# Kernel optimization log

Measured on AMD Instinct MI355X. Metric: run time of the kernel, lower is better.

Reference implementation:

```python
import jax, jax.numpy as jnp
import numpy as np

B, S, D = 4, 4096, 256


def setup_inputs() -> dict:
    key = jax.random.key(0)
    ks = jax.random.split(key, 7)
    s = 1.0 / np.sqrt(D)
    return {
        "x": jax.random.normal(ks[0], (B, S, D), dtype=jnp.float32),
        "Wq": jax.random.normal(ks[1], (D, D), dtype=jnp.float32) * s,
        "bq": jax.random.normal(ks[2], (D,), dtype=jnp.float32) * s,
        "Wk": jax.random.normal(ks[3], (D, D), dtype=jnp.float32) * s,
        "bk": jax.random.normal(ks[4], (D,), dtype=jnp.float32) * s,
        "Wv": jax.random.normal(ks[5], (D, D), dtype=jnp.float32) * s,
        "bv": jax.random.normal(ks[6], (D,), dtype=jnp.float32) * s,
    }


def reference(x, Wq, bq, Wk, bk, Wv, bv):
    # QKV projections (torch Linear: y = x @ W^T + b; here W stored as [in, out])
    Q = jax.nn.relu(jnp.einsum("bsd,df->bsf", x, Wq) + bq)  # [B,S,D]
    K = jax.nn.relu(jnp.einsum("bsd,df->bsf", x, Wk) + bk)  # [B,S,D]
    V = jnp.einsum("bsd,df->bsf", x, Wv) + bv               # [B,S,D]
    scores = jnp.einsum("bqd,bkd->bqk", Q, K)               # [B,S,S], no 1/sqrt(d) scaling (as in source)
    attn = jax.nn.softmax(scores, axis=-1)
    return jnp.einsum("bqk,bkd->bqd", attn, V)              # [B,S,D]
```

## Files before the change

kernel.cpp:

```cpp
#include <hip/hip_runtime.h>
#include <stdint.h>

typedef __bf16 bf16;
typedef bf16 bf16x8 __attribute__((ext_vector_type(8)));
typedef _Float16 f16;
typedef f16 f16x8 __attribute__((ext_vector_type(8)));
typedef f16 f16x4 __attribute__((ext_vector_type(4)));
typedef float f32x4 __attribute__((ext_vector_type(4)));
typedef float f32x16 __attribute__((ext_vector_type(16)));
typedef unsigned short u16;
typedef unsigned int u32;
typedef u32 u32x2 __attribute__((ext_vector_type(2)));
typedef u16 u16x8v __attribute__((ext_vector_type(8)));

__device__ __forceinline__ u16 f2bf(float f) {
  u32 u = __float_as_uint(f);
  u32 r = u + 0x7fffu + ((u >> 16) & 1u);
  return (u16)(r >> 16);
}
__device__ __forceinline__ float bf2f(u16 h) { return __uint_as_float(((u32)h) << 16); }

__device__ __forceinline__ u32 pkrtz(float a, float b) {
  auto r = __builtin_amdgcn_cvt_pkrtz(a, b);
  u32 u; __builtin_memcpy(&u, &r, 4);
  return u;
}

union ABu { u16x8v u; bf16x8 b; };
union PAu { u32 w[4]; f16x8 v; };

__global__ void wt_kernel(const float* __restrict__ Wq, const float* __restrict__ Wk,
                          const float* __restrict__ Wv, u16* __restrict__ Wh,
                          u16* __restrict__ Wl) {
  int w = blockIdx.x >> 4;
  int chunk = blockIdx.x & 15;
  const float* W = (w == 0) ? Wq : (w == 1) ? Wk : Wv;
  int t = threadIdx.x;
  int o = chunk * 16 + (t & 15);
  int i0 = (t >> 4) * 16;
  u16x8v h0, h1, l0, l1;
  #pragma unroll
  for (int ii = 0; ii < 8; ++ii) {
    float v0 = W[(size_t)(i0 + ii) * 256 + o];
    u16 h = f2bf(v0); h0[ii] = h; l0[ii] = f2bf(v0 - bf2f(h));
    float v1 = W[(size_t)(i0 + 8 + ii) * 256 + o];
    h = f2bf(v1); h1[ii] = h; l1[ii] = f2bf(v1 - bf2f(h));
  }
  size_t base = (size_t)w * 65536 + (size_t)o * 256 + i0;
  *(u16x8v*)(Wh + base) = h0; *(u16x8v*)(Wh + base + 8) = h1;
  *(u16x8v*)(Wl + base) = l0; *(u16x8v*)(Wl + base + 8) = l1;
}

__global__ __launch_bounds__(256, 2) void proj_kernel(
    const float* __restrict__ x, const float* __restrict__ bq,
    const float* __restrict__ bk, const float* __restrict__ bv,
    const u16* __restrict__ Wh, const u16* __restrict__ Wl,
    f16* __restrict__ Qf, f16* __restrict__ Kf, f16* __restrict__ Vt) {
  __shared__ __align__(16) char Whs[16384];
  __shared__ __align__(16) char Wls[16384];

  int m = blockIdx.x, w = blockIdx.y;
  int tid = threadIdx.x, lane = tid & 63, wv = tid >> 6;
  int r = lane & 15, c = lane >> 4;
  int row0 = m * 128 + wv * 32;
  const char* Whw = (const char*)(Wh + (size_t)w * 65536);
  const char* Wlw = (const char*)(Wl + (size_t)w * 65536);
  const float* bias = (w == 0) ? bq : (w == 1) ? bk : bv;

  f32x4 acc[2][16];
  #pragma unroll
  for (int g = 0; g < 2; ++g)
    #pragma unroll
    for (int n = 0; n < 16; ++n) acc[g][n] = (f32x4)0.0f;

  for (int ks = 0; ks < 8; ++ks) {
    if (ks) __syncthreads();
    #pragma unroll
    for (int ss = 0; ss < 4; ++ss) {
      int slot = ss * 256 + tid;
      int row = slot >> 2, c4 = slot & 3;
      int dby = (c4 << 4) ^ (((row >> 1) & 3) << 4);
      const char* gh = Whw + (size_t)row * 512 + ks * 64 + dby;
      const char* gl = Wlw + (size_t)row * 512 + ks * 64 + dby;
      __builtin_amdgcn_global_load_lds(
          (const __attribute__((address_space(1))) void*)gh,
          (__attribute__((address_space(3))) void*)(Whs + slot * 16), 16, 0, 0);
      __builtin_amdgcn_global_load_lds(
          (const __attribute__((address_space(1))) void*)gl,
          (__attribute__((address_space(3))) void*)(Wls + slot * 16), 16, 0, 0);
    }
    __syncthreads();

    ABu ah[2], al[2];
    #pragma unroll
    for (int g = 0; g < 2; ++g) {
      const float* xrow = x + (size_t)(row0 + g * 16 + r) * 256 + ks * 32 + c * 8;
      float4 a0 = *(const float4*)(xrow);
      float4 a1 = *(const float4*)(xrow + 4);
      float xv[8] = {a0.x, a0.y, a0.z, a0.w, a1.x, a1.y, a1.z, a1.w};
      #pragma unroll
      for (int j = 0; j < 8; ++j) {
        u16 h = f2bf(xv[j]);
        ah[g].u[j] = h;
        al[g].u[j] = f2bf(xv[j] - bf2f(h));
      }
    }
    #pragma unroll
    for (int n = 0; n < 16; ++n) {
      int wrow = n * 16 + r;
      int wof = (c * 16) ^ (((wrow >> 1) & 3) << 4);
      bf16x8 whf = *(const bf16x8*)(Whs + wrow * 64 + wof);
      bf16x8 wlf = *(const bf16x8*)(Wls + wrow * 64 + wof);
      #pragma unroll
      for (int g = 0; g < 2; ++g) {
        acc[g][n] = __builtin_amdgcn_mfma_f32_16x16x32_bf16(ah[g].b, whf, acc[g][n], 0, 0, 0);
        acc[g][n] = __builtin_amdgcn_mfma_f32_16x16x32_bf16(al[g].b, whf, acc[g][n], 0, 0, 0);
        acc[g][n] = __builtin_amdgcn_mfma_f32_16x16x32_bf16(ah[g].b, wlf, acc[g][n], 0, 0, 0);
      }
    }
  }

  if (w < 2) {
    f16* outp = (w == 0) ? Qf : Kf;
    #pragma unroll
    for (int g = 0; g < 2; ++g)
      #pragma unroll
      for (int n = 0; n < 16; ++n) {
        int col = n * 16 + r;
        float bb = bias[col];
        #pragma unroll
        for (int i = 0; i < 4; ++i) {
          float v = fmaxf(acc[g][n][i] + bb, 0.0f);
          outp[(size_t)(row0 + g * 16 + c * 4 + i) * 256 + col] = (f16)v;
        }
      }
  } else {
    #pragma unroll
    for (int g = 0; g < 2; ++g) {
      int grow = row0 + g * 16 + c * 4;
      int b = grow >> 12, s0 = grow & 4095;
      #pragma unroll
      for (int n = 0; n < 16; ++n) {
        int d = n * 16 + r;
        float bb = bias[d];
        f16x4 pk;
        #pragma unroll
        for (int i = 0; i < 4; ++i) pk[i] = (f16)(acc[g][n][i] + bb);
        *(f16x4*)(Vt + (size_t)(b * 256 + d) * 4096 + s0) = pk;
      }
    }
  }
}

__global__ __launch_bounds__(256, 2) void attn_kernel(
    const f16* __restrict__ Qf, const f16* __restrict__ Kf,
    const f16* __restrict__ Vt, f16* __restrict__ Opart, float* __restrict__ Ml) {
  __shared__ __align__(16) char Ksm[2][16384];
  __shared__ __align__(16) char Vsm[3][16384];

  int bid = blockIdx.x;
  int xcd = bid & 7;
  int batch = xcd >> 1;
  int kq = ((xcd & 1) << 1) | ((bid >> 3) & 1);
  int qtl = bid >> 4;
  int tid = threadIdx.x, lane = tid & 63, wv = tid >> 6;
  int ln = lane & 31, hi = lane >> 5;
  int q0 = qtl * 128 + wv * 32;
  int kv0 = kq * 1024;

  f16x8 qf[16];
  {
    const f16* qp = Qf + ((size_t)(batch * 4096 + q0 + ln)) * 256 + hi * 8;
    #pragma unroll
    for (int ks = 0; ks < 16; ++ks) qf[ks] = *(const f16x8*)(qp + ks * 16);
  }

  f32x16 O[8];
  #pragma unroll
  for (int dt = 0; dt < 8; ++dt) O[dt] = (f32x16)0.0f;
  float m_ = -1.0e30f, l_ = 0.0f;
  PAu pa0_, pa1_;

  const char* Kbase = (const char*)(Kf + ((size_t)(batch * 4096 + kv0)) * 256);
  const char* Vbase = (const char*)(Vt + (size_t)batch * 1048576 + kv0);

#define STAGE(T, KB, VB)                                                       \
  {                                                                            \
    _Pragma("unroll")                                                          \
    for (int rr = 0; rr < 4; ++rr) {                                           \
      int slot = rr * 256 + tid;                                               \
      int krow = slot >> 5;                                                    \
      int dby = ((slot & 31) << 4) ^ ((krow & 7) << 4);                        \
      const char* g = Kbase + (size_t)((T) * 32 + krow) * 512 + dby;           \
      __builtin_amdgcn_global_load_lds(                                        \
          (const __attribute__((address_space(1))) void*)g,                    \
          (__attribute__((address_space(3))) void*)(Ksm[KB] + slot * 16), 16, 0, 0); \
    }                                                                          \
    _Pragma("unroll")                                                          \
    for (int rr = 0; rr < 4; ++rr) {                                           \
      int slot = rr * 256 + tid;                                               \
      int vrow = slot >> 2;                                                    \
      int dby = ((slot & 3) << 4) ^ (((vrow >> 1) & 3) << 4);                  \
      const char* g = Vbase + (size_t)vrow * 8192 + (T) * 64 + dby;            \
      __builtin_amdgcn_global_load_lds(                                        \
          (const __attribute__((address_space(1))) void*)g,                    \
          (__attribute__((address_space(3))) void*)(Vsm[VB] + slot * 16), 16, 0, 0); \
    }                                                                          \
  }

  int kswz = (ln & 7) << 4;
  int vswz = ((ln >> 1) & 3) << 4;
  int hi16 = hi * 16;

#define QKPV(T, DOPV)                                                          \
  {                                                                            \
    const char* Kc = Ksm[(T) & 1];                                             \
    const char* Vc = Vsm[((T) + 2) % 3];                                       \
    f32x16 sA = (f32x16)0.0f;                                                  \
    __builtin_amdgcn_s_setprio(1);                                             \
    _Pragma("unroll")                                                          \
    for (int ks = 0; ks < 16; ++ks) {                                          \
      f16x8 kf = *(const f16x8*)(Kc + ln * 512 + ((ks * 32 + hi16) ^ kswz));   \
      sA = __builtin_amdgcn_mfma_f32_32x32x16_f16(kf, qf[ks], sA, 0, 0, 0);    \
      if (DOPV) {                                                              \
        int dt = ks >> 1, half = ks & 1;                                       \
        f16x8 vf = *(const f16x8*)(Vc + (dt * 32 + ln) * 64 +                  \
                                   ((half * 32 + hi16) ^ vswz));               \
        O[dt] = __builtin_amdgcn_mfma_f32_32x32x16_f16(                        \
            half ? pa1_.v : pa0_.v, vf, O[dt], 0, 0, 0);                       \
      }                                                                        \
    }                                                                          \
    __builtin_amdgcn_s_setprio(0);                                             \
    float pm = fmaxf(                                                          \
        fmaxf(fmaxf(fmaxf(sA[0], sA[1]), fmaxf(sA[2], sA[3])),                 \
              fmaxf(fmaxf(sA[4], sA[5]), fmaxf(sA[6], sA[7]))),                \
        fmaxf(fmaxf(fmaxf(sA[8], sA[9]), fmaxf(sA[10], sA[11])),               \
              fmaxf(fmaxf(sA[12], sA[13]), fmaxf(sA[14], sA[15]))));           \
    pm = fmaxf(pm, __shfl_xor(pm, 32));                                        \
    if (!__all(pm <= m_ + 8.0f)) {                                             \
      float mn = fmaxf(m_, pm);                                                \
      float sc = __expf(m_ - mn);                                              \
      m_ = mn; l_ *= sc;                                                       \
      _Pragma("unroll")                                                        \
      for (int rg = 0; rg < 16; ++rg) {                                        \
        float srg = __shfl(sc, (rg & 3) + 8 * (rg >> 2) + 4 * hi);             \
        _Pragma("unroll")                                                      \
        for (int dt = 0; dt < 8; ++dt) O[dt][rg] *= srg;                       \
      }                                                                        \
    }                                                                          \
    float p_[16];                                                              \
    _Pragma("unroll")                                                          \
    for (int j = 0; j < 16; ++j) p_[j] = __expf(sA[j] - m_);                   \
    float ps = (((p_[0] + p_[1]) + (p_[2] + p_[3])) +                          \
                ((p_[4] + p_[5]) + (p_[6] + p_[7]))) +                         \
               (((p_[8] + p_[9]) + (p_[10] + p_[11])) +                        \
                ((p_[12] + p_[13]) + (p_[14] + p_[15])));                      \
    ps += __shfl_xor(ps, 32);                                                  \
    l_ += ps;                                                                  \
    {                                                                          \
      u32x2 r1 = __builtin_amdgcn_permlane32_swap(pkrtz(p_[0], p_[1]), pkrtz(p_[4], p_[5]), false, false); \
      u32x2 r2 = __builtin_amdgcn_permlane32_swap(pkrtz(p_[2], p_[3]), pkrtz(p_[6], p_[7]), false, false); \
      pa0_.w[0] = r1[0]; pa0_.w[1] = r2[0]; pa0_.w[2] = r1[1]; pa0_.w[3] = r2[1]; \
      u32x2 r3 = __builtin_amdgcn_permlane32_swap(pkrtz(p_[8], p_[9]), pkrtz(p_[12], p_[13]), false, false); \
      u32x2 r4 = __builtin_amdgcn_permlane32_swap(pkrtz(p_[10], p_[11]), pkrtz(p_[14], p_[15]), false, false); \
      pa1_.w[0] = r3[0]; pa1_.w[1] = r4[0]; pa1_.w[2] = r3[1]; pa1_.w[3] = r4[1]; \
    }                                                                          \
  }

  STAGE(0, 0, 0);
  STAGE(1, 1, 1);
  asm volatile("s_waitcnt vmcnt(8)" ::: "memory");
  __builtin_amdgcn_sched_barrier(0);
  __builtin_amdgcn_s_barrier();
  QKPV(0, false);

  for (int t = 1; t < 32; ++t) {
    __builtin_amdgcn_s_barrier();
    if (t < 31) {
      int kb = (t + 1) & 1, vb = (t + 1) % 3;
      STAGE(t + 1, kb, vb);
      asm volatile("s_waitcnt vmcnt(8)" ::: "memory");
    } else {
      asm volatile("s_waitcnt vmcnt(0)" ::: "memory");
    }
    __builtin_amdgcn_sched_barrier(0);
    __builtin_amdgcn_s_barrier();
    QKPV(t, true);
  }

  {
    const char* Vc = Vsm[31 % 3];
    #pragma unroll
    for (int ks = 0; ks < 16; ++ks) {
      int dt = ks >> 1, half = ks & 1;
      f16x8 vf = *(const f16x8*)(Vc + (dt * 32 + ln) * 64 + ((half * 32 + hi16) ^ vswz));
      O[dt] = __builtin_amdgcn_mfma_f32_32x32x16_f16(half ? pa1_.v : pa0_.v, vf, O[dt], 0, 0, 0);
    }
  }

  float invl = 1.0f / l_;
  #pragma unroll
  for (int rg = 0; rg < 16; ++rg) {
    int qr = (rg & 3) + 8 * (rg >> 2) + 4 * hi;
    float iv = __shfl(invl, qr);
    size_t row = (size_t)kq * 16384 + batch * 4096 + q0 + qr;
    #pragma unroll
    for (int dt = 0; dt < 8; ++dt)
      Opart[row * 256 + dt * 32 + ln] = (f16)(O[dt][rg] * iv);
  }
  if (hi == 0) {
    size_t grow = (size_t)kq * 16384 + batch * 4096 + q0 + ln;
    Ml[grow * 2] = m_;
    Ml[grow * 2 + 1] = l_;
  }
#undef STAGE
#undef QKPV
}

__global__ __launch_bounds__(256) void merge_kernel(
    const f16* __restrict__ Opart, const float* __restrict__ Ml,
    float* __restrict__ out) {
  int gid = blockIdx.x * 256 + threadIdx.x;
  int row = gid >> 5, d0 = (gid & 31) * 8;
  float m[4], l[4];
  #pragma unroll
  for (int p = 0; p < 4; ++p) {
    m[p] = Ml[((size_t)p * 16384 + row) * 2];
    l[p] = Ml[((size_t)p * 16384 + row) * 2 + 1];
  }
  float M = fmaxf(fmaxf(m[0], m[1]), fmaxf(m[2], m[3]));
  float wl[4], L = 0.f;
  #pragma unroll
  for (int p = 0; p < 4; ++p) { wl[p] = __expf(m[p] - M) * l[p]; L += wl[p]; }
  float o[8] = {0.f, 0.f, 0.f, 0.f, 0.f, 0.f, 0.f, 0.f};
  #pragma unroll
  for (int p = 0; p < 4; ++p) {
    f16x8 v = *(const f16x8*)(Opart + ((size_t)p * 16384 + row) * 256 + d0);
    #pragma unroll
    for (int j = 0; j < 8; ++j) o[j] += wl[p] * (float)v[j];
  }
  float invL = 1.0f / L;
  float4 o0 = {o[0] * invL, o[1] * invL, o[2] * invL, o[3] * invL};
  float4 o1 = {o[4] * invL, o[5] * invL, o[6] * invL, o[7] * invL};
  *(float4*)(out + (size_t)row * 256 + d0) = o0;
  *(float4*)(out + (size_t)row * 256 + d0 + 4) = o1;
}

extern "C" void kernel_launch(void* const* d_in, const int* in_sizes, int n_in,
                              void* d_out, int out_size, void* d_ws, size_t ws_size,
                              hipStream_t stream) {
  const float* x  = (const float*)d_in[0];
  const float* Wq = (const float*)d_in[1];
  const float* bq = (const float*)d_in[2];
  const float* Wk = (const float*)d_in[3];
  const float* bk = (const float*)d_in[4];
  const float* Wv = (const float*)d_in[5];
  const float* bv = (const float*)d_in[6];
  float* out = (float*)d_out;

  u16* Wh = (u16*)d_ws;
  u16* Wl = Wh + 3 * 65536;
  f16* Qf = (f16*)(Wl + 3 * 65536);
  f16* Kf = Qf + (size_t)16384 * 256;
  f16* Vt = Kf + (size_t)16384 * 256;
  f16* Opart = Vt + (size_t)4 * 256 * 4096;
  float* Ml = (float*)(Opart + (size_t)4 * 16384 * 256);

  wt_kernel<<<48, 256, 0, stream>>>(Wq, Wk, Wv, Wh, Wl);
  proj_kernel<<<dim3(128, 3), 256, 0, stream>>>(x, bq, bk, bv, Wh, Wl, Qf, Kf, Vt);
  attn_kernel<<<512, 256, 0, stream>>>(Qf, Kf, Vt, Opart, Ml);
  merge_kernel<<<2048, 256, 0, stream>>>(Opart, Ml, out);
}
```

Before: 168.2 us.

## Enlarge attention blocks to 8 waves with 64-key tiles and double buffering

The attention kernel now launches 256 blocks of 512 threads, each covering 256 query rows and sharing 64-key K/V tiles in LDS. This halves the number of barriers and stages per key range. The V buffers change from triple to double buffering with a new 128-byte row swizzle. Within each tile, the two 32-key halves are software pipelined, so the PV MMA of the first half is interleaved with the QK MMA of the second half. The cost is twice the LDS per block (128KB) and fewer, larger blocks, which may reduce occupancy and overlap across the CUs.

Measured after the change: 157.4 us. 1.07x faster.

```diff
diff --git a/kernel.cpp b/kernel.cpp
--- a/kernel.cpp
+++ b/kernel.cpp
@@ -152,11 +152,11 @@
   }
 }
 
-__global__ __launch_bounds__(256, 2) void attn_kernel(
+__global__ __launch_bounds__(512, 2) void attn_kernel(
     const f16* __restrict__ Qf, const f16* __restrict__ Kf,
     const f16* __restrict__ Vt, f16* __restrict__ Opart, float* __restrict__ Ml) {
-  __shared__ __align__(16) char Ksm[2][16384];
-  __shared__ __align__(16) char Vsm[3][16384];
+  __shared__ __align__(16) char Ksm[2][32768];
+  __shared__ __align__(16) char Vsm[2][32768];
 
   int bid = blockIdx.x;
   int xcd = bid & 7;
@@ -165,7 +165,7 @@
   int qtl = bid >> 4;
   int tid = threadIdx.x, lane = tid & 63, wv = tid >> 6;
   int ln = lane & 31, hi = lane >> 5;
-  int q0 = qtl * 128 + wv * 32;
+  int q0 = qtl * 256 + wv * 32;
   int kv0 = kq * 1024;
 
   f16x8 qf[16];
@@ -179,63 +179,45 @@
   #pragma unroll
   for (int dt = 0; dt < 8; ++dt) O[dt] = (f32x16)0.0f;
   float m_ = -1.0e30f, l_ = 0.0f;
-  PAu pa0_, pa1_;
 
   const char* Kbase = (const char*)(Kf + ((size_t)(batch * 4096 + kv0)) * 256);
   const char* Vbase = (const char*)(Vt + (size_t)batch * 1048576 + kv0);
 
-#define STAGE(T, KB, VB)                                                       \
+#define STAGE(T, BF)                                                           \
   {                                                                            \
     _Pragma("unroll")                                                          \
     for (int rr = 0; rr < 4; ++rr) {                                           \
-      int slot = rr * 256 + tid;                                               \
+      int slot = rr * 512 + tid;                                               \
       int krow = slot >> 5;                                                    \
       int dby = ((slot & 31) << 4) ^ ((krow & 7) << 4);                        \
-      const char* g = Kbase + (size_t)((T) * 32 + krow) * 512 + dby;           \
+      const char* g = Kbase + (size_t)((T) * 64 + krow) * 512 + dby;           \
       __builtin_amdgcn_global_load_lds(                                        \
           (const __attribute__((address_space(1))) void*)g,                    \
-          (__attribute__((address_space(3))) void*)(Ksm[KB] + slot * 16), 16, 0, 0); \
+          (__attribute__((address_space(3))) void*)(Ksm[BF] + slot * 16), 16, 0, 0); \
     }                                                                          \
     _Pragma("unroll")                                                          \
     for (int rr = 0; rr < 4; ++rr) {                                           \
-      int slot = rr * 256 + tid;                                               \
-      int vrow = slot >> 2;                                                    \
-      int dby = ((slot & 3) << 4) ^ (((vrow >> 1) & 3) << 4);                  \
-      const char* g = Vbase + (size_t)vrow * 8192 + (T) * 64 + dby;            \
+      int slot = rr * 512 + tid;                                               \
+      int vrow = slot >> 3;                                                    \
+      int dby = ((slot & 7) << 4) ^ ((vrow & 7) << 4);                         \
+      const char* g = Vbase + (size_t)vrow * 8192 + (T) * 128 + dby;           \
       __builtin_amdgcn_global_load_lds(                                        \
           (const __attribute__((address_space(1))) void*)g,                    \
-          (__attribute__((address_space(3))) void*)(Vsm[VB] + slot * 16), 16, 0, 0); \
+          (__attribute__((address_space(3))) void*)(Vsm[BF] + slot * 16), 16, 0, 0); \
     }                                                                          \
   }
 
   int kswz = (ln & 7) << 4;
-  int vswz = ((ln >> 1) & 3) << 4;
+  int vswz = (ln & 7) << 4;
   int hi16 = hi * 16;
 
-#define QKPV(T, DOPV)                                                          \
+#define SOFTMAX(SA, PA0, PA1)                                                  \
   {                                                                            \
-    const char* Kc = Ksm[(T) & 1];                                             \
-    const char* Vc = Vsm[((T) + 2) % 3];                                       \
-    f32x16 sA = (f32x16)0.0f;                                                  \
-    __builtin_amdgcn_s_setprio(1);                                             \
-    _Pragma("unroll")                                                          \
-    for (int ks = 0; ks < 16; ++ks) {                                          \
-      f16x8 kf = *(const f16x8*)(Kc + ln * 512 + ((ks * 32 + hi16) ^ kswz));   \
-      sA = __builtin_amdgcn_mfma_f32_32x32x16_f16(kf, qf[ks], sA, 0, 0, 0);    \
-      if (DOPV) {                                                              \
-        int dt = ks >> 1, half = ks & 1;                                       \
-        f16x8 vf = *(const f16x8*)(Vc + (dt * 32 + ln) * 64 +                  \
-                                   ((half * 32 + hi16) ^ vswz));               \
-        O[dt] = __builtin_amdgcn_mfma_f32_32x32x16_f16(                        \
-            half ? pa1_.v : pa0_.v, vf, O[dt], 0, 0, 0);                       \
-      }                                                                        \
-    }                                                                          \
-    __builtin_amdgcn_s_setprio(0);                                             \
     float pm = fmaxf(                                                          \
-        fmaxf(fmaxf(fmaxf(sA[0], sA[1]), fmaxf(sA[2], sA[3])),                 \
-              fmaxf(fmaxf(sA[4], sA[5]), fmaxf(sA[6], sA[7]))),                \
-        fmaxf(fmaxf(fmaxf(sA[8], sA[9]), fmaxf(sA[10], sA[11])),               \
-              fmaxf(fmaxf(sA[12], sA[13]), fmaxf(sA[14], sA[15]))));           \
+        fmaxf(fmaxf(fmaxf(SA[0], SA[1]), fmaxf(SA[2], SA[3])),                 \
+              fmaxf(fmaxf(SA[4], SA[5]), fmaxf(SA[6], SA[7]))),                \
+        fmaxf(fmaxf(fmaxf(SA[8], SA[9]), fmaxf(SA[10], SA[11])),               \
+              fmaxf(fmaxf(SA[12], SA[13]), fmaxf(SA[14], SA[15]))));           \
     pm = fmaxf(pm, __shfl_xor(pm, 32));                                        \
     if (!__all(pm <= m_ + 8.0f)) {                                             \
       float mn = fmaxf(m_, pm);                                                \
@@ -250,7 +232,7 @@
     }                                                                          \
     float p_[16];                                                              \
     _Pragma("unroll")                                                          \
-    for (int j = 0; j < 16; ++j) p_[j] = __expf(sA[j] - m_);                   \
+    for (int j = 0; j < 16; ++j) p_[j] = __expf(SA[j] - m_);                   \
     float ps = (((p_[0] + p_[1]) + (p_[2] + p_[3])) +                          \
                 ((p_[4] + p_[5]) + (p_[6] + p_[7]))) +                         \
                (((p_[8] + p_[9]) + (p_[10] + p_[11])) +                        \
@@ -260,42 +242,62 @@
     {                                                                          \
       u32x2 r1 = __builtin_amdgcn_permlane32_swap(pkrtz(p_[0], p_[1]), pkrtz(p_[4], p_[5]), false, false); \
       u32x2 r2 = __builtin_amdgcn_permlane32_swap(pkrtz(p_[2], p_[3]), pkrtz(p_[6], p_[7]), false, false); \
-      pa0_.w[0] = r1[0]; pa0_.w[1] = r2[0]; pa0_.w[2] = r1[1]; pa0_.w[3] = r2[1]; \
+      PA0.w[0] = r1[0]; PA0.w[1] = r2[0]; PA0.w[2] = r1[1]; PA0.w[3] = r2[1];  \
       u32x2 r3 = __builtin_amdgcn_permlane32_swap(pkrtz(p_[8], p_[9]), pkrtz(p_[12], p_[13]), false, false); \
       u32x2 r4 = __builtin_amdgcn_permlane32_swap(pkrtz(p_[10], p_[11]), pkrtz(p_[14], p_[15]), false, false); \
-      pa1_.w[0] = r3[0]; pa1_.w[1] = r4[0]; pa1_.w[2] = r3[1]; pa1_.w[3] = r4[1]; \
+      PA1.w[0] = r3[0]; PA1.w[1] = r4[0]; PA1.w[2] = r3[1]; PA1.w[3] = r4[1];  \
     }                                                                          \
   }
 
-  STAGE(0, 0, 0);
-  STAGE(1, 1, 1);
-  asm volatile("s_waitcnt vmcnt(8)" ::: "memory");
-  __builtin_amdgcn_sched_barrier(0);
-  __builtin_amdgcn_s_barrier();
-  QKPV(0, false);
-
-  for (int t = 1; t < 32; ++t) {
+  STAGE(0, 0);
+
+  for (int t = 0; t < 16; ++t) {
     __builtin_amdgcn_s_barrier();
-    if (t < 31) {
-      int kb = (t + 1) & 1, vb = (t + 1) % 3;
-      STAGE(t + 1, kb, vb);
+    if (t < 15) {
+      STAGE(t + 1, (t + 1) & 1);
       asm volatile("s_waitcnt vmcnt(8)" ::: "memory");
     } else {
       asm volatile("s_waitcnt vmcnt(0)" ::: "memory");
     }
     __builtin_amdgcn_sched_barrier(0);
     __builtin_amdgcn_s_barrier();
-    QKPV(t, true);
-  }
-
-  {
-    const char* Vc = Vsm[31 % 3];
+
+    const char* Kc = Ksm[t & 1];
+    const char* Vc = Vsm[t & 1];
+
+    f32x16 sA = (f32x16)0.0f;
+    __builtin_amdgcn_s_setprio(1);
     #pragma unroll
     for (int ks = 0; ks < 16; ++ks) {
-      int dt = ks >> 1, half = ks & 1;
-      f16x8 vf = *(const f16x8*)(Vc + (dt * 32 + ln) * 64 + ((half * 32 + hi16) ^ vswz));
-      O[dt] = __builtin_amdgcn_mfma_f32_32x32x16_f16(half ? pa1_.v : pa0_.v, vf, O[dt], 0, 0, 0);
-    }
+      f16x8 kf = *(const f16x8*)(Kc + ln * 512 + ((ks * 32 + hi16) ^ kswz));
+      sA = __builtin_amdgcn_mfma_f32_32x32x16_f16(kf, qf[ks], sA, 0, 0, 0);
+    }
+    __builtin_amdgcn_s_setprio(0);
+    PAu paA0, paA1;
+    SOFTMAX(sA, paA0, paA1);
+
+    f32x16 sB = (f32x16)0.0f;
+    __builtin_amdgcn_s_setprio(1);
+    #pragma unroll
+    for (int ks = 0; ks < 16; ++ks) {
+      f16x8 kf = *(const f16x8*)(Kc + (32 + ln) * 512 + ((ks * 32 + hi16) ^ kswz));
+      sB = __builtin_amdgcn_mfma_f32_32x32x16_f16(kf, qf[ks], sB, 0, 0, 0);
+      int dt = ks >> 1, k2 = ks & 1;
+      f16x8 vf = *(const f16x8*)(Vc + (dt * 32 + ln) * 128 + ((k2 * 32 + hi16) ^ vswz));
+      O[dt] = __builtin_amdgcn_mfma_f32_32x32x16_f16(k2 ? paA1.v : paA0.v, vf, O[dt], 0, 0, 0);
+    }
+    __builtin_amdgcn_s_setprio(0);
+    PAu paB0, paB1;
+    SOFTMAX(sB, paB0, paB1);
+
+    __builtin_amdgcn_s_setprio(1);
+    #pragma unroll
+    for (int ks = 0; ks < 16; ++ks) {
+      int dt = ks >> 1, k2 = ks & 1;
+      f16x8 vf = *(const f16x8*)(Vc + (dt * 32 + ln) * 128 + ((64 + k2 * 32 + hi16) ^ vswz));
+      O[dt] = __builtin_amdgcn_mfma_f32_32x32x16_f16(k2 ? paB1.v : paB0.v, vf, O[dt], 0, 0, 0);
+    }
+    __builtin_amdgcn_s_setprio(0);
   }
 
   float invl = 1.0f / l_;
@@ -314,7 +316,7 @@
     Ml[grow * 2 + 1] = l_;
   }
 #undef STAGE
-#undef QKPV
+#undef SOFTMAX
 }
 
 __global__ __launch_bounds__(256) void merge_kernel(
@@ -368,6 +370,6 @@
 
   wt_kernel<<<48, 256, 0, stream>>>(Wq, Wk, Wv, Wh, Wl);
   proj_kernel<<<dim3(128, 3), 256, 0, stream>>>(x, bq, bk, bv, Wh, Wl, Qf, Kf, Vt);
-  attn_kernel<<<512, 256, 0, stream>>>(Qf, Kf, Vt, Opart, Ml);
+  attn_kernel<<<256, 512, 0, stream>>>(Qf, Kf, Vt, Opart, Ml);
   merge_kernel<<<2048, 256, 0, stream>>>(Opart, Ml, out);
 }
```
